# Kernel tuning notes

Measured on AMD Instinct MI355X. Metric: run time of the kernel, lower is better.

## Reference

```python
import jax, jax.numpy as jnp
import numpy as np

B, S, C = 4, 2048, 1024

def setup_inputs() -> dict:
    key = jax.random.key(0)
    ks = jax.random.split(key, 9)
    lim = 1.0 / np.sqrt(C)  # torch nn.Linear default init range
    def lin_params(kw, kb):
        W = jax.random.uniform(kw, (C, C), jnp.float32, -lim, lim)
        b = jax.random.uniform(kb, (C,), jnp.float32, -lim, lim)
        return W, b
    Wq, bq = lin_params(ks[0], ks[1])
    Wk, bk = lin_params(ks[2], ks[3])
    Wv, bv = lin_params(ks[4], ks[5])
    query = jax.random.normal(ks[6], (B, S, C), jnp.float32)
    key_t = jax.random.normal(ks[7], (B, S, C), jnp.float32)
    value = jax.random.normal(ks[8], (B, S, C), jnp.float32)
    return {"query": query, "key": key_t, "value": value,
            "Wq": Wq, "bq": bq, "Wk": Wk, "bk": bk, "Wv": Wv, "bv": bv}

def reference(query, key, value, Wq, bq, Wk, bk, Wv, bv):
    # Linear projections: y = x @ W^T + b (torch Linear convention, W is [out, in])
    Q = jnp.einsum('bsc,dc->bsd', query, Wq) + bq
    K = jnp.einsum('bsc,dc->bsd', key, Wk) + bk
    V = jnp.einsum('bsc,dc->bsd', value, Wv) + bv
    scale = jnp.float32(C) ** 0.5
    scores = jnp.einsum('bqd,bkd->bqk', Q, K) / scale  # [B, S, S]
    attn = jax.nn.softmax(scores, axis=-1)
    out = jnp.einsum('bqk,bkd->bqd', attn, V)  # [B, S, C]
    return out
```

## Files before the change

kernel.cpp:

```cpp
#include <hip/hip_runtime.h>
#include <hip/hip_bf16.h>


typedef _Float16 half8 __attribute__((ext_vector_type(8)));
typedef _Float16 half4 __attribute__((ext_vector_type(4)));
typedef float f32x4 __attribute__((ext_vector_type(4)));

#define AS1(p) ((const __attribute__((address_space(1))) void*)(p))
#define AS3(p) ((__attribute__((address_space(3))) void*)(p))
#define MFMA16(a, b, c) __builtin_amdgcn_mfma_f32_16x16x32_f16(a, b, c, 0, 0, 0)

__global__ __launch_bounds__(256) void cvt3_f32_f16(
    const float* __restrict__ s0, const float* __restrict__ s1,
    const float* __restrict__ s2, _Float16* __restrict__ d0,
    _Float16* __restrict__ d1, _Float16* __restrict__ d2, int n) {
    const float* s = blockIdx.y == 0 ? s0 : blockIdx.y == 1 ? s1 : s2;
    _Float16* d = blockIdx.y == 0 ? d0 : blockIdx.y == 1 ? d1 : d2;
    int i = (blockIdx.x * 256 + threadIdx.x) * 8;
    if (i >= n) return;
    float4 a = *(const float4*)(s + i);
    float4 b = *(const float4*)(s + i + 4);
    half8 h;
    h[0] = (_Float16)a.x; h[1] = (_Float16)a.y; h[2] = (_Float16)a.z; h[3] = (_Float16)a.w;
    h[4] = (_Float16)b.x; h[5] = (_Float16)b.y; h[6] = (_Float16)b.z; h[7] = (_Float16)b.w;
    *(half8*)(d + i) = h;
}

template <int K, int NX_SH, int R, int NYT_SH, bool BIAS, bool F16OUT, bool PROJ3>
__global__ __launch_bounds__(256, 2)
void gemm_nt(const _Float16* __restrict__ A, const _Float16* __restrict__ Bt,
             const float* __restrict__ b0, const float* __restrict__ b1,
             const float* __restrict__ b2, void* __restrict__ Cout,
             _Float16* __restrict__ VtOut, int N, float scale,
             long sA, long sB, long sC) {
    __shared__ _Float16 Asm[128 * 64] __attribute__((aligned(16)));
    __shared__ _Float16 Bsm[128 * 64] __attribute__((aligned(16)));
    const int tid = threadIdx.x;
    const int lane = tid & 63;
    const int wave = tid >> 6;

    const int lin = blockIdx.x;
    const int g = lin & 7;
    const int s = lin >> 3;
    const int xt = s & ((1 << NX_SH) - 1);
    const int row_id = g * R + (s >> NX_SH);
    const int yt = row_id & ((1 << NYT_SH) - 1);
    const int tz = row_id >> NYT_SH;
    const int m0 = yt * 128;
    const int n0 = xt * 128;

    const float* bias = nullptr;
    if constexpr (PROJ3) {
        A += (long)tz * 8388608;
        Bt += (long)tz * 1048576;
        bias = tz == 0 ? b0 : tz == 1 ? b1 : b2;
    } else {
        A += (long)tz * sA;
        Bt += (long)tz * sB;
    }

    const int srow8 = lane >> 3;
    const int sq = ((lane & 7) ^ srow8) << 3;
    const int quad = lane >> 4;
    const int l16 = lane & 15;
    const int wm = (wave >> 1) << 6;
    const int wn = (wave & 1) << 6;
    const int fa0 = (wm + l16) * 64 + (((0 * 4 + quad) ^ (l16 & 7)) << 3);
    const int fa1 = (wm + l16) * 64 + (((1 * 4 + quad) ^ (l16 & 7)) << 3);
    const int fb0 = (wn + l16) * 64 + (((0 * 4 + quad) ^ (l16 & 7)) << 3);
    const int fb1 = (wn + l16) * 64 + (((1 * 4 + quad) ^ (l16 & 7)) << 3);

    f32x4 acc[4][4];
#pragma unroll
    for (int i = 0; i < 4; i++)
#pragma unroll
        for (int j = 0; j < 4; j++)
#pragma unroll
            for (int r = 0; r < 4; r++) acc[i][j][r] = 0.0f;

    const _Float16* Abase = A + (long)m0 * K;
    const _Float16* Bbase = Bt + (long)n0 * K;

    for (int k0 = 0; k0 < K; k0 += 64) {
        __syncthreads();
#pragma unroll
        for (int u = 0; u < 8; ++u) {
            const int t = wave + u * 4;
            if (t < 16) {
                __builtin_amdgcn_global_load_lds(
                    AS1(Abase + (long)(t * 8 + srow8) * K + k0 + sq),
                    AS3(Asm + t * 512), 16, 0, 0);
            } else {
                __builtin_amdgcn_global_load_lds(
                    AS1(Bbase + (long)((t - 16) * 8 + srow8) * K + k0 + sq),
                    AS3(Bsm + (t - 16) * 512), 16, 0, 0);
            }
        }
        __syncthreads();

#pragma unroll
        for (int ks = 0; ks < 2; ++ks) {
            const int ao = ks ? fa1 : fa0;
            const int bo = ks ? fb1 : fb0;
            half8 af[4], bf[4];
#pragma unroll
            for (int i = 0; i < 4; i++) af[i] = *(const half8*)(Asm + ao + i * 1024);
#pragma unroll
            for (int j = 0; j < 4; j++) bf[j] = *(const half8*)(Bsm + bo + j * 1024);
#pragma unroll
            for (int i = 0; i < 4; i++)
#pragma unroll
                for (int j = 0; j < 4; j++)
                    acc[i][j] = MFMA16(af[i], bf[j], acc[i][j]);
        }
    }

    const bool trout = PROJ3 && tz == 2;
#pragma unroll
    for (int i = 0; i < 4; i++) {
        const int row = m0 + wm + i * 16 + quad * 4;
#pragma unroll
        for (int j = 0; j < 4; j++) {
            const int col = n0 + wn + j * 16 + l16;
            const float badd = BIAS ? bias[col] : 0.0f;
            if (trout) {
                const long b = row >> 11;
                const int sl = row & 2047;
                half4 h;
#pragma unroll
                for (int r = 0; r < 4; r++) h[r] = (_Float16)(acc[i][j][r] * scale + badd);
                *(half4*)(VtOut + b * 2097152 + (long)col * 2048 + sl) = h;
            } else if constexpr (PROJ3) {
                _Float16* o = (_Float16*)Cout + (long)tz * 8388608;
#pragma unroll
                for (int r = 0; r < 4; r++)
                    o[(long)(row + r) * N + col] = (_Float16)(acc[i][j][r] * scale + badd);
            } else {
#pragma unroll
                for (int r = 0; r < 4; r++) {
                    float v = acc[i][j][r] * scale + badd;
                    if constexpr (F16OUT)
                        ((_Float16*)Cout + (long)tz * sC)[(long)(row + r) * N + col] = (_Float16)v;
                    else
                        ((float*)Cout + (long)tz * sC)[(long)(row + r) * N + col] = v;
                }
            }
        }
    }
}

template <int K, int NX_SH, int R, int NYT_SH, bool BIAS, bool F16OUT, bool PROJ3>
__global__ __launch_bounds__(512, 2)
void gemm256(const _Float16* __restrict__ A, const _Float16* __restrict__ Bt,
             const float* __restrict__ b0, const float* __restrict__ b1,
             const float* __restrict__ b2, void* __restrict__ Cout,
             _Float16* __restrict__ VtOut, int N, float scale,
             long sA, long sB, long sC) {
    constexpr int NT = K / 64;
    static_assert(NT >= 2, "need >=2 K-tiles");
    __shared__ _Float16 sm[2][2][256 * 64] __attribute__((aligned(16)));

    const int tid = threadIdx.x;
    const int lane = tid & 63;
    const int wave = tid >> 6;
    const int wm_i = wave >> 2;
    const int wn_i = wave & 3;

    const int lin = blockIdx.x;
    const int g = lin & 7;
    const int sblk = lin >> 3;
    const int xt = sblk & ((1 << NX_SH) - 1);
    const int row_id = g * R + (sblk >> NX_SH);
    const int yt = row_id & ((1 << NYT_SH) - 1);
    const int tz = row_id >> NYT_SH;
    const int m0 = yt * 256;
    const int n0 = xt * 256;

    const float* bias = nullptr;
    if constexpr (PROJ3) {
        A += (long)tz * 8388608;
        Bt += (long)tz * 1048576;
        bias = tz == 0 ? b0 : tz == 1 ? b1 : b2;
    } else {
        A += (long)tz * sA;
        Bt += (long)tz * sB;
    }
    const _Float16* Abase = A + (long)m0 * K;
    const _Float16* Bbase = Bt + (long)n0 * K;

    const int srow8 = lane >> 3;
    const int sq = ((lane & 7) ^ srow8) << 3;
    const int quad = lane >> 4;
    const int l16 = lane & 15;
    const int e7 = l16 & 7;
    const int ch0 = (quad ^ e7) << 3;
    const int ch1 = ((4 + quad) ^ e7) << 3;
    const int arow = (wm_i * 128 + l16) * 64;
    const int brow = (wn_i * 64 + l16) * 64;

    f32x4 acc[8][4];
#pragma unroll
    for (int i = 0; i < 8; i++)
#pragma unroll
        for (int j = 0; j < 4; j++)
#pragma unroll
            for (int r = 0; r < 4; r++) acc[i][j][r] = 0.0f;

    auto STAGE = [&](int bfi, int ab, int half, int kt) {
        const _Float16* gb = ab ? Bbase : Abase;
#pragma unroll
        for (int u = 0; u < 2; ++u) {
            const int c8 = (u << 3) + wave;
            const int r = half * 128 + c8 * 8 + srow8;
            __builtin_amdgcn_global_load_lds(
                AS1(gb + (long)r * K + kt * 64 + sq),
                AS3(&sm[bfi][ab][half * 8192 + c8 * 512]), 16, 0, 0);
        }
    };

    STAGE(0, 0, 0, 0);
    STAGE(0, 0, 1, 0);
    STAGE(0, 1, 0, 0);
    STAGE(0, 1, 1, 0);
    STAGE(1, 1, 0, 1);
    STAGE(1, 1, 1, 1);
    asm volatile("s_waitcnt vmcnt(4)" ::: "memory");
    __builtin_amdgcn_s_barrier();

    half8 af[4][2], bfr[4][2];
#pragma unroll 2
    for (int t = 0; t < NT; ++t) {
        const int c = t & 1;
        const int nb = c ^ 1;
        const _Float16* sAp = sm[c][0];
        const _Float16* sBp = sm[c][1];

#pragma unroll
        for (int i = 0; i < 4; ++i) {
            af[i][0] = *(const half8*)(sAp + arow + i * 1024 + ch0);
            af[i][1] = *(const half8*)(sAp + arow + i * 1024 + ch1);
        }
#pragma unroll
        for (int j = 0; j < 2; ++j) {
            bfr[j][0] = *(const half8*)(sBp + brow + j * 1024 + ch0);
            bfr[j][1] = *(const half8*)(sBp + brow + j * 1024 + ch1);
        }
        if (t + 1 < NT) STAGE(nb, 0, 0, t + 1);
        __builtin_amdgcn_s_barrier();
        asm volatile("s_waitcnt lgkmcnt(0)" ::: "memory");
        __builtin_amdgcn_s_setprio(1);
#pragma unroll
        for (int i = 0; i < 4; ++i)
#pragma unroll
            for (int j = 0; j < 2; ++j) {
                acc[i][j] = MFMA16(af[i][0], bfr[j][0], acc[i][j]);
                acc[i][j] = MFMA16(af[i][1], bfr[j][1], acc[i][j]);
            }
        __builtin_amdgcn_s_setprio(0);
        __builtin_amdgcn_s_barrier();

#pragma unroll
        for (int j = 2; j < 4; ++j) {
            bfr[j][0] = *(const half8*)(sBp + brow + j * 1024 + ch0);
            bfr[j][1] = *(const half8*)(sBp + brow + j * 1024 + ch1);
        }
        if (t + 1 < NT) STAGE(nb, 0, 1, t + 1);
        __builtin_amdgcn_s_barrier();
        asm volatile("s_waitcnt lgkmcnt(0)" ::: "memory");
        __builtin_amdgcn_s_setprio(1);
#pragma unroll
        for (int i = 0; i < 4; ++i)
#pragma unroll
            for (int j = 2; j < 4; ++j) {
                acc[i][j] = MFMA16(af[i][0], bfr[j][0], acc[i][j]);
                acc[i][j] = MFMA16(af[i][1], bfr[j][1], acc[i][j]);
            }
        __builtin_amdgcn_s_setprio(0);
        __builtin_amdgcn_s_barrier();

#pragma unroll
        for (int i = 0; i < 4; ++i) {
            af[i][0] = *(const half8*)(sAp + arow + (i + 4) * 1024 + ch0);
            af[i][1] = *(const half8*)(sAp + arow + (i + 4) * 1024 + ch1);
        }
        if (t + 2 < NT) STAGE(c, 1, 0, t + 2);
        __builtin_amdgcn_s_barrier();
        asm volatile("s_waitcnt lgkmcnt(0)" ::: "memory");
        __builtin_amdgcn_s_setprio(1);
#pragma unroll
        for (int i = 0; i < 4; ++i)
#pragma unroll
            for (int j = 0; j < 2; ++j) {
                acc[i + 4][j] = MFMA16(af[i][0], bfr[j][0], acc[i + 4][j]);
                acc[i + 4][j] = MFMA16(af[i][1], bfr[j][1], acc[i + 4][j]);
            }
        __builtin_amdgcn_s_setprio(0);
        __builtin_amdgcn_s_barrier();

        if (t + 2 < NT) STAGE(c, 1, 1, t + 2);
        __builtin_amdgcn_s_barrier();
        __builtin_amdgcn_s_setprio(1);
#pragma unroll
        for (int i = 0; i < 4; ++i)
#pragma unroll
            for (int j = 2; j < 4; ++j) {
                acc[i + 4][j] = MFMA16(af[i][0], bfr[j][0], acc[i + 4][j]);
                acc[i + 4][j] = MFMA16(af[i][1], bfr[j][1], acc[i + 4][j]);
            }
        __builtin_amdgcn_s_setprio(0);
        if (t + 2 < NT)
            asm volatile("s_waitcnt vmcnt(4)" ::: "memory");
        else
            asm volatile("s_waitcnt vmcnt(0)" ::: "memory");
        __builtin_amdgcn_s_barrier();
    }

    const bool trout = PROJ3 && tz == 2;
#pragma unroll
    for (int i = 0; i < 8; ++i) {
        const int row = m0 + wm_i * 128 + i * 16 + quad * 4;
#pragma unroll
        for (int j = 0; j < 4; ++j) {
            const int col = n0 + wn_i * 64 + j * 16 + l16;
            const float badd = BIAS ? bias[col] : 0.0f;
            if (trout) {
                const long b = row >> 11;
                const int sl = row & 2047;
                half4 h;
#pragma unroll
                for (int r = 0; r < 4; r++) h[r] = (_Float16)(acc[i][j][r] * scale + badd);
                *(half4*)(VtOut + b * 2097152 + (long)col * 2048 + sl) = h;
            } else if constexpr (PROJ3) {
                _Float16* o = (_Float16*)Cout + (long)tz * 8388608;
#pragma unroll
                for (int r = 0; r < 4; r++)
                    o[(long)(row + r) * N + col] = (_Float16)(acc[i][j][r] * scale + badd);
            } else {
#pragma unroll
                for (int r = 0; r < 4; r++) {
                    float v = acc[i][j][r] * scale + badd;
                    if constexpr (F16OUT)
                        ((_Float16*)Cout + (long)tz * sC)[(long)(row + r) * N + col] = (_Float16)v;
                    else
                        ((float*)Cout + (long)tz * sC)[(long)(row + r) * N + col] = v;
                }
            }
        }
    }
}

__global__ __launch_bounds__(256) void softmax_f16(const _Float16* __restrict__ S,
                                                   _Float16* __restrict__ P) {
    const long row = blockIdx.x;
    const int t = threadIdx.x;
    const int wave = t >> 6, lane = t & 63;
    half8 h = ((const half8*)(S + row * 2048))[t];
    float v[8];
#pragma unroll
    for (int j = 0; j < 8; j++) v[j] = (float)h[j];
    float m = v[0];
#pragma unroll
    for (int j = 1; j < 8; j++) m = fmaxf(m, v[j]);
#pragma unroll
    for (int off = 32; off > 0; off >>= 1) m = fmaxf(m, __shfl_xor(m, off, 64));
    __shared__ float redm[4], reds[4];
    if (lane == 0) redm[wave] = m;
    __syncthreads();
    m = fmaxf(fmaxf(redm[0], redm[1]), fmaxf(redm[2], redm[3]));
    float sum = 0.0f;
#pragma unroll
    for (int j = 0; j < 8; j++) { v[j] = __expf(v[j] - m); sum += v[j]; }
#pragma unroll
    for (int off = 32; off > 0; off >>= 1) sum += __shfl_xor(sum, off, 64);
    if (lane == 0) reds[wave] = sum;
    __syncthreads();
    sum = (reds[0] + reds[1]) + (reds[2] + reds[3]);
    const float inv = 1.0f / sum;
    half8 o;
#pragma unroll
    for (int j = 0; j < 8; j++) o[j] = (_Float16)(v[j] * inv);
    ((half8*)(P + row * 2048))[t] = o;
}

extern "C" void kernel_launch(void* const* d_in, const int* in_sizes, int n_in,
                              void* d_out, int out_size, void* d_ws, size_t ws_size,
                              hipStream_t stream) {
    constexpr int B = 4, S = 2048, C = 1024;
    constexpr long XSZ = (long)B * S * C;
    constexpr long WSZ = (long)C * C;

    const float* query = (const float*)d_in[0];
    const float* key   = (const float*)d_in[1];
    const float* value = (const float*)d_in[2];
    const float* Wq = (const float*)d_in[3];
    const float* bq = (const float*)d_in[4];
    const float* Wk = (const float*)d_in[5];
    const float* bk = (const float*)d_in[6];
    const float* Wv = (const float*)d_in[7];
    const float* bv = (const float*)d_in[8];
    float* out = (float*)d_out;
    char* ws = (char*)d_ws;

    _Float16* Xq  = (_Float16*)(ws + 0);
    _Float16* Wqh = (_Float16*)(ws + 3 * XSZ * 2);
    _Float16* scores = (_Float16*)(ws + 0);
    _Float16* Qh  = (_Float16*)(ws + 73400320);
    _Float16* attn = (_Float16*)(ws + 73400320);
    _Float16* Vt  = (_Float16*)(ws + 106954752);
    if (ws_size < 123731968) return;

    cvt3_f32_f16<<<dim3(XSZ / 2048, 3), 256, 0, stream>>>(
        query, key, value, Xq, Xq + XSZ, Xq + 2 * XSZ, (int)XSZ);
    cvt3_f32_f16<<<dim3(WSZ / 2048, 3), 256, 0, stream>>>(
        Wq, Wk, Wv, Wqh, Wqh + WSZ, Wqh + 2 * WSZ, (int)WSZ);

    gemm256<1024, 2, 12, 5, true, true, true><<<384, 512, 0, stream>>>(
        Xq, Wqh, bq, bk, bv, Qh, Vt, C, 1.0f, 0, 0, 0);

    gemm256<1024, 3, 4, 3, false, true, false><<<256, 512, 0, stream>>>(
        Qh, Qh + XSZ, nullptr, nullptr, nullptr, scores, nullptr, S, 0.03125f,
        (long)S * C, (long)S * C, (long)S * S);

    softmax_f16<<<B * S, 256, 0, stream>>>(scores, attn);

    gemm_nt<2048, 3, 8, 4, false, false, false><<<512, 256, 0, stream>>>(
        attn, Vt, nullptr, nullptr, nullptr, out, nullptr, C, 1.0f,
        (long)S * S, (long)C * S, (long)S * C);
}
```

Baseline: 320.4 us.

## Restructure GEMM main loop to hold all A fragments and prefetch deeper

Reorders the 256x256 GEMM inner loop so each wave keeps all eight A fragments in registers and iterates B in two halves. The A tile for the next K-step is staged earlier, and most of the mid-loop workgroup barriers are removed, with sched_barrier fences added to hold the order. The goal is to cut barrier stalls and overlap more global-to-LDS traffic with MFMA work. The cost is more register pressure and a more delicate LDS buffer reuse schedule, where a mistake could cause a race or a miscomputed vmcnt.

```diff
diff --git a/kernel.cpp b/kernel.cpp
--- a/kernel.cpp
+++ b/kernel.cpp
@@ -157,7 +157,7 @@
              _Float16* __restrict__ VtOut, int N, float scale,
              long sA, long sB, long sC) {
     constexpr int NT = K / 64;
-    static_assert(NT >= 2, "need >=2 K-tiles");
+    static_assert(NT >= 3, "prologue needs >=3 K-tiles");
     __shared__ _Float16 sm[2][2][256 * 64] __attribute__((aligned(16)));
 
     const int tid = threadIdx.x;
@@ -222,12 +222,13 @@
     STAGE(0, 0, 1, 0);
     STAGE(0, 1, 0, 0);
     STAGE(0, 1, 1, 0);
+    STAGE(1, 0, 0, 1);
+    STAGE(1, 0, 1, 1);
     STAGE(1, 1, 0, 1);
-    STAGE(1, 1, 1, 1);
-    asm volatile("s_waitcnt vmcnt(4)" ::: "memory");
+    asm volatile("s_waitcnt vmcnt(6)" ::: "memory");
     __builtin_amdgcn_s_barrier();
 
-    half8 af[4][2], bfr[4][2];
+    half8 af[8][2], bfr[2][2];
 #pragma unroll 2
     for (int t = 0; t < NT; ++t) {
         const int c = t & 1;
@@ -245,9 +246,9 @@
             bfr[j][0] = *(const half8*)(sBp + brow + j * 1024 + ch0);
             bfr[j][1] = *(const half8*)(sBp + brow + j * 1024 + ch1);
         }
-        if (t + 1 < NT) STAGE(nb, 0, 0, t + 1);
-        __builtin_amdgcn_s_barrier();
+        if (t + 1 < NT) STAGE(nb, 1, 1, t + 1);
         asm volatile("s_waitcnt lgkmcnt(0)" ::: "memory");
+        __builtin_amdgcn_sched_barrier(0);
         __builtin_amdgcn_s_setprio(1);
 #pragma unroll
         for (int i = 0; i < 4; ++i)
@@ -257,21 +258,19 @@
                 acc[i][j] = MFMA16(af[i][1], bfr[j][1], acc[i][j]);
             }
         __builtin_amdgcn_s_setprio(0);
-        __builtin_amdgcn_s_barrier();
-
-#pragma unroll
-        for (int j = 2; j < 4; ++j) {
-            bfr[j][0] = *(const half8*)(sBp + brow + j * 1024 + ch0);
-            bfr[j][1] = *(const half8*)(sBp + brow + j * 1024 + ch1);
-        }
-        if (t + 1 < NT) STAGE(nb, 0, 1, t + 1);
-        __builtin_amdgcn_s_barrier();
+
+#pragma unroll
+        for (int i = 4; i < 8; ++i) {
+            af[i][0] = *(const half8*)(sAp + arow + i * 1024 + ch0);
+            af[i][1] = *(const half8*)(sAp + arow + i * 1024 + ch1);
+        }
         asm volatile("s_waitcnt lgkmcnt(0)" ::: "memory");
+        __builtin_amdgcn_sched_barrier(0);
         __builtin_amdgcn_s_setprio(1);
 #pragma unroll
-        for (int i = 0; i < 4; ++i)
-#pragma unroll
-            for (int j = 2; j < 4; ++j) {
+        for (int i = 4; i < 8; ++i)
+#pragma unroll
+            for (int j = 0; j < 2; ++j) {
                 acc[i][j] = MFMA16(af[i][0], bfr[j][0], acc[i][j]);
                 acc[i][j] = MFMA16(af[i][1], bfr[j][1], acc[i][j]);
             }
@@ -279,38 +278,40 @@
         __builtin_amdgcn_s_barrier();
 
 #pragma unroll
-        for (int i = 0; i < 4; ++i) {
-            af[i][0] = *(const half8*)(sAp + arow + (i + 4) * 1024 + ch0);
-            af[i][1] = *(const half8*)(sAp + arow + (i + 4) * 1024 + ch1);
-        }
-        if (t + 2 < NT) STAGE(c, 1, 0, t + 2);
-        __builtin_amdgcn_s_barrier();
+        for (int j = 0; j < 2; ++j) {
+            bfr[j][0] = *(const half8*)(sBp + brow + (j + 2) * 1024 + ch0);
+            bfr[j][1] = *(const half8*)(sBp + brow + (j + 2) * 1024 + ch1);
+        }
+        if (t + 2 < NT) {
+            STAGE(c, 0, 0, t + 2);
+            STAGE(c, 0, 1, t + 2);
+        }
         asm volatile("s_waitcnt lgkmcnt(0)" ::: "memory");
+        __builtin_amdgcn_sched_barrier(0);
         __builtin_amdgcn_s_setprio(1);
 #pragma unroll
         for (int i = 0; i < 4; ++i)
 #pragma unroll
             for (int j = 0; j < 2; ++j) {
-                acc[i + 4][j] = MFMA16(af[i][0], bfr[j][0], acc[i + 4][j]);
-                acc[i + 4][j] = MFMA16(af[i][1], bfr[j][1], acc[i + 4][j]);
+                acc[i][j + 2] = MFMA16(af[i][0], bfr[j][0], acc[i][j + 2]);
+                acc[i][j + 2] = MFMA16(af[i][1], bfr[j][1], acc[i][j + 2]);
             }
         __builtin_amdgcn_s_setprio(0);
         __builtin_amdgcn_s_barrier();
 
-        if (t + 2 < NT) STAGE(c, 1, 1, t + 2);
-        __builtin_amdgcn_s_barrier();
+        if (t + 2 < NT) STAGE(c, 1, 0, t + 2);
         __builtin_amdgcn_s_setprio(1);
 #pragma unroll
-        for (int i = 0; i < 4; ++i)
-#pragma unroll
-            for (int j = 2; j < 4; ++j) {
-                acc[i + 4][j] = MFMA16(af[i][0], bfr[j][0], acc[i + 4][j]);
-                acc[i + 4][j] = MFMA16(af[i][1], bfr[j][1], acc[i + 4][j]);
+        for (int i = 4; i < 8; ++i)
+#pragma unroll
+            for (int j = 0; j < 2; ++j) {
+                acc[i][j + 2] = MFMA16(af[i][0], bfr[j][0], acc[i][j + 2]);
+                acc[i][j + 2] = MFMA16(af[i][1], bfr[j][1], acc[i][j + 2]);
             }
         __builtin_amdgcn_s_setprio(0);
         if (t + 2 < NT)
-            asm volatile("s_waitcnt vmcnt(4)" ::: "memory");
-        else
+            asm volatile("s_waitcnt vmcnt(6)" ::: "memory");
+        else if (t + 1 < NT)
             asm volatile("s_waitcnt vmcnt(0)" ::: "memory");
         __builtin_amdgcn_s_barrier();
     }
```

Measured after the change: 306.3 us. -4.4%, faster.
